# Optimization experiments

Hardware: AMD Instinct MI355X
Metric: run time of the kernel (lower is better)

The kernel has to match this reference:

```python
import jax, jax.numpy as jnp
import numpy as np

DIM = 768
D_STATE = 16
D_INNER = 2 * DIM  # expand=2


def setup_inputs() -> dict:
    key = jax.random.key(0)
    k_x, k_in, k_conv, k_out = jax.random.split(key, 4)
    B, L = 1, 4096
    x = jax.random.normal(k_x, (B, L, DIM), dtype=jnp.float32)
    # torch Linear weight layout: [out_features, in_features]
    W_in = jax.random.normal(k_in, (3 * D_INNER + 2 * D_STATE, DIM), dtype=jnp.float32) * 0.02
    # depthwise conv1d kernel: [out_ch=d_inner, in_ch/groups=1, k=3]
    W_conv = jax.random.normal(k_conv, (D_INNER, 1, 3), dtype=jnp.float32) * 0.1
    W_out = jax.random.normal(k_out, (DIM, D_INNER), dtype=jnp.float32) * 0.02
    A_log = jnp.log(jnp.tile(jnp.arange(1, D_STATE + 1, dtype=jnp.float32), (D_INNER, 1)))
    D = jnp.ones((D_INNER,), dtype=jnp.float32)
    return {"x": x, "W_in": W_in, "W_conv": W_conv, "W_out": W_out, "A_log": A_log, "D": D}


def reference(x, W_in, W_conv, W_out, A_log, D):
    d_inner = W_conv.shape[0]
    d_state = A_log.shape[1]
    Bsz = x.shape[0]

    xz = x @ W_in.T  # [B, L, 3*d_inner + 2*d_state]
    x_inner, z, B_ssm, C_ssm, delta = jnp.split(
        xz, [d_inner, 2 * d_inner, 2 * d_inner + d_state, 2 * d_inner + 2 * d_state], axis=-1
    )

    # depthwise conv over sequence: [B, d_inner, L]
    xc = jax.lax.conv_general_dilated(
        x_inner.transpose(0, 2, 1), W_conv,
        window_strides=(1,), padding=[(1, 1)], feature_group_count=d_inner,
    ).transpose(0, 2, 1)  # back to [B, L, d_inner]
    xc = jax.nn.silu(xc)

    A = -jnp.exp(A_log)  # [d_inner, d_state]
    delta = jax.nn.softplus(delta)  # [B, L, d_inner]
    dA = jnp.exp(jnp.einsum('bld,dn->bldn', delta, A))           # [B, L, d_inner, d_state]
    dBx = jnp.einsum('bld,bln,bld->bldn', delta, B_ssm, xc)      # delta_B * x fused

    def step(h, inp):
        da_t, dbx_t, c_t = inp  # [B,d,n], [B,d,n], [B,n]
        h = da_t * h + dbx_t
        y_t = jnp.einsum('bdn,bn->bd', h, c_t)
        return h, y_t

    h0 = jnp.zeros((Bsz, d_inner, d_state), dtype=x.dtype)
    _, ys = jax.lax.scan(
        step, h0,
        (dA.transpose(1, 0, 2, 3), dBx.transpose(1, 0, 2, 3), C_ssm.transpose(1, 0, 2)),
    )  # ys: [L, B, d_inner]

    y = ys.transpose(1, 0, 2) + xc * D  # skip connection
    y = y * jax.nn.silu(z)
    return y @ W_out.T  # [B, L, dim]
```

## Files before the change

### kernel.cpp

```cpp
#include <hip/hip_runtime.h>
#include <hip/hip_bf16.h>
#include <math.h>

#define LSEQ   4096
#define DIM    768
#define DINNER 1536
#define DSTATE 16
#define NCOLS  4640
#define NCH    128
#define CLEN   32
#define NPAD   4736

typedef _Float16 f16;
typedef __attribute__((ext_vector_type(8))) _Float16 f16x8;
typedef __attribute__((ext_vector_type(4))) float f32x4;

#define WSCALE   64.0f
#define WDESCALE 0.015625f

__device__ __forceinline__ void gld_lds16(void* lds_dst, const void* gsrc) {
    __builtin_amdgcn_global_load_lds(
        (__attribute__((address_space(1))) void*)(gsrc),
        (__attribute__((address_space(3))) void*)(lds_dst), 16, 0, 0);
}

template<int BM, int BN, int WM, int WN, int NTB, bool COLM, bool SPLIT, bool ZMODE>
__global__ __launch_bounds__(256) void gemm_f16(const f16* __restrict__ A,
                                                const f16* __restrict__ B,
                                                float* __restrict__ C,
                                                f16* __restrict__ Z,
                                                int M, int N, int K, int ldc,
                                                float cscale) {
    constexpr int MI  = WM / 16;
    constexpr int NI  = WN / 16;
    constexpr int NWN = BN / WN;
    constexpr int nA  = BM / 16;
    constexpr int nB  = BN / 16;
    constexpr int NPL = SPLIT ? 2 : 1;
    constexpr int NT  = nA + NPL * nB;

    __shared__ __align__(16) f16 As[BM * 32];
    __shared__ __align__(16) f16 Bs[NPL * BN * 32];

    const int P   = gridDim.x >> 3;
    const int idx = (blockIdx.x & 7) * P + (blockIdx.x >> 3);
    const int m0  = (COLM ? (idx % NTB) : (idx / NTB)) * BM;
    const int n0  = (COLM ? (idx / NTB) : (idx % NTB)) * BN;

    const int tid  = threadIdx.x;
    const int w    = tid >> 6;
    const int lane = tid & 63;
    const int wr   = w / NWN;
    const int wc   = w % NWN;
    const int m    = lane & 15;
    const int q    = lane >> 4;
    const int rsub = lane >> 2;
    const int bsel = lane & 3;
    const int ldb  = NPL * K;

    f32x4 acc[MI][NI];
#pragma unroll
    for (int i = 0; i < MI; i++)
#pragma unroll
        for (int j = 0; j < NI; j++) acc[i][j] = (f32x4){0.f, 0.f, 0.f, 0.f};

    const int fragoff = ((q ^ (m & 3)) << 3);

    for (int k0 = 0; k0 < K; k0 += 32) {
#pragma unroll
        for (int t = w; t < NT; t += 4) {
            const f16* g; f16* lb; int rl;
            if (t < nA) {
                rl = t * 16 + rsub;
                g  = A + (size_t)(m0 + rl) * K + k0 + (bsel ^ (rl & 3)) * 8;
                lb = As + t * 16 * 32;
            } else if (t < nA + nB) {
                int tt = t - nA; rl = tt * 16 + rsub;
                g  = B + (size_t)(n0 + rl) * ldb + k0 + (bsel ^ (rl & 3)) * 8;
                lb = Bs + tt * 16 * 32;
            } else {
                int tt = t - nA - nB; rl = tt * 16 + rsub;
                g  = B + (size_t)(n0 + rl) * ldb + K + k0 + (bsel ^ (rl & 3)) * 8;
                lb = Bs + (nB + tt) * 16 * 32;
            }
            gld_lds16(lb, g);
        }
        __syncthreads();

        f16x8 af[MI], bh[NI];
#pragma unroll
        for (int i = 0; i < MI; i++)
            af[i] = *(const f16x8*)&As[(wr * WM + i * 16 + m) * 32 + fragoff];
#pragma unroll
        for (int j = 0; j < NI; j++)
            bh[j] = *(const f16x8*)&Bs[(wc * WN + j * 16 + m) * 32 + fragoff];
#pragma unroll
        for (int i = 0; i < MI; i++)
#pragma unroll
            for (int j = 0; j < NI; j++)
                acc[i][j] = __builtin_amdgcn_mfma_f32_16x16x32_f16(af[i], bh[j], acc[i][j], 0, 0, 0);
        if (SPLIT) {
            f16x8 bl[NI];
#pragma unroll
            for (int j = 0; j < NI; j++)
                bl[j] = *(const f16x8*)&Bs[BN * 32 + (wc * WN + j * 16 + m) * 32 + fragoff];
#pragma unroll
            for (int i = 0; i < MI; i++)
#pragma unroll
                for (int j = 0; j < NI; j++)
                    acc[i][j] = __builtin_amdgcn_mfma_f32_16x16x32_f16(af[i], bl[j], acc[i][j], 0, 0, 0);
        }
        __syncthreads();
    }

    if (ZMODE && n0 >= DINNER && n0 < 2 * DINNER) {
#pragma unroll
        for (int i = 0; i < MI; i++) {
#pragma unroll
            for (int j = 0; j < NI; j++) {
                const int col = n0 - DINNER + wc * WN + j * 16 + m;
                const int rowb = m0 + wr * WM + i * 16 + q * 4;
#pragma unroll
                for (int r = 0; r < 4; r++)
                    Z[(size_t)(rowb + r) * DINNER + col] = (f16)acc[i][j][r];
            }
        }
        return;
    }
#pragma unroll
    for (int i = 0; i < MI; i++) {
#pragma unroll
        for (int j = 0; j < NI; j++) {
            const int col = n0 + wc * WN + j * 16 + m;
            if (col >= N) continue;
            const int rowb = m0 + wr * WM + i * 16 + q * 4;
#pragma unroll
            for (int r = 0; r < 4; r++)
                C[(size_t)(rowb + r) * ldc + col] = acc[i][j][r] * cscale;
        }
    }
}

#define E0 (LSEQ * DIM)
#define E1 (E0 + NPAD * DIM)
#define E2 (E1 + DIM * DINNER)

__global__ __launch_bounds__(256) void cvt_all(const float* __restrict__ x,
                                               const float* __restrict__ Wi,
                                               const float* __restrict__ Wo,
                                               f16* __restrict__ Ax,
                                               f16* __restrict__ Bw,
                                               f16* __restrict__ Bo) {
    int i = (blockIdx.x * 256 + threadIdx.x) * 4;
    if (i < E0) {
        float4 v = *(const float4*)(x + i);
        Ax[i] = (f16)v.x; Ax[i+1] = (f16)v.y; Ax[i+2] = (f16)v.z; Ax[i+3] = (f16)v.w;
    } else if (i < E1) {
        int e = i - E0;
        int n = e / DIM;
        if (n < NCOLS) {
            float4 v = *(const float4*)(Wi + e);
            Bw[e] = (f16)v.x; Bw[e+1] = (f16)v.y; Bw[e+2] = (f16)v.z; Bw[e+3] = (f16)v.w;
        } else {
            Bw[e] = (f16)0.f; Bw[e+1] = (f16)0.f; Bw[e+2] = (f16)0.f; Bw[e+3] = (f16)0.f;
        }
    } else if (i < E2) {
        int e = i - E1;
        int n = e / DINNER, k = e - n * DINNER;
        float4 v = *(const float4*)(Wo + e);
        float a[4] = {v.x * WSCALE, v.y * WSCALE, v.z * WSCALE, v.w * WSCALE};
        f16* row = Bo + (size_t)n * (2 * DINNER) + k;
#pragma unroll
        for (int j = 0; j < 4; j++) {
            f16 hi = (f16)a[j];
            row[j] = hi; row[DINNER + j] = (f16)(a[j] - (float)hi);
        }
    }
}

__global__ __launch_bounds__(256) void scan1_kernel(const float* __restrict__ xz,
                                                    const float* __restrict__ Wc,
                                                    const float* __restrict__ A_log,
                                                    float* __restrict__ aprod,
                                                    float* __restrict__ hend) {
    __shared__ float Bs[CLEN * DSTATE];
    const int d  = blockIdx.x * 256 + threadIdx.x;
    const int c  = blockIdx.y;
    const int l0 = c * CLEN;
    for (int i = threadIdx.x; i < CLEN * DSTATE; i += 256)
        Bs[i] = xz[(size_t)(l0 + (i >> 4)) * NCOLS + 3072 + (i & 15)];
    float Areg[DSTATE];
#pragma unroll
    for (int n = 0; n < DSTATE; n++) Areg[n] = -__expf(A_log[d * DSTATE + n]);
    const float w0 = Wc[d * 3 + 0], w1 = Wc[d * 3 + 1], w2 = Wc[d * 3 + 2];
    float xm = (l0 > 0) ? xz[(size_t)(l0 - 1) * NCOLS + d] : 0.f;
    float x0 = xz[(size_t)l0 * NCOLS + d];
    float ld_xp   = xz[(size_t)(l0 + 1) * NCOLS + d];
    float ld_draw = xz[(size_t)l0 * NCOLS + 3104 + d];
    __syncthreads();

    float h[DSTATE];
#pragma unroll
    for (int n = 0; n < DSTATE; n++) h[n] = 0.f;
    float S = 0.f;

    for (int t = 0; t < CLEN; t++) {
        const int l = l0 + t;
        float xp = ld_xp, draw = ld_draw;
        if (t + 1 < CLEN) {
            ld_xp   = (l + 2 < LSEQ) ? xz[(size_t)(l + 2) * NCOLS + d] : 0.f;
            ld_draw = xz[(size_t)(l + 1) * NCOLS + 3104 + d];
        }
        float v  = xm * w0 + x0 * w1 + xp * w2;
        float xcv = __fdividef(v, 1.f + __expf(-v));
        float dtv = (draw > 20.f) ? draw : __logf(1.f + __expf(draw));
        float u = dtv * xcv;
        S += dtv;
#pragma unroll
        for (int n = 0; n < DSTATE; n++) {
            float e = __expf(dtv * Areg[n]);
            h[n] = e * h[n] + u * Bs[t * DSTATE + n];
        }
        xm = x0; x0 = xp;
    }
#pragma unroll
    for (int n = 0; n < DSTATE; n++) {
        size_t idx = ((size_t)c * DSTATE + n) * DINNER + d;
        aprod[idx] = __expf(S * Areg[n]);
        hend[idx]  = h[n];
    }
}

__global__ __launch_bounds__(256) void scan2_kernel(const float* __restrict__ aprod,
                                                    const float* __restrict__ hend,
                                                    float* __restrict__ hinit) {
    const int g = blockIdx.x * 256 + threadIdx.x;
    const size_t S = (size_t)DSTATE * DINNER;
    size_t idx = g;
    float a = aprod[idx], e = hend[idx];
    float h = 0.f;
#pragma unroll 4
    for (int c = 0; c < NCH; c++) {
        float ac = a, ec = e;
        if (c + 1 < NCH) { a = aprod[idx + S]; e = hend[idx + S]; }
        hinit[idx] = h;
        h = ac * h + ec;
        idx += S;
    }
}

__global__ __launch_bounds__(256) void scan3_kernel(const float* __restrict__ xz,
                                                    const f16* __restrict__ Zb,
                                                    const float* __restrict__ Wc,
                                                    const float* __restrict__ A_log,
                                                    const float* __restrict__ hinit,
                                                    const float* __restrict__ Dp,
                                                    f16* __restrict__ Ay) {
    __shared__ float Bs[CLEN * DSTATE];
    __shared__ float Cs[CLEN * DSTATE];
    const int d  = blockIdx.x * 256 + threadIdx.x;
    const int c  = blockIdx.y;
    const int l0 = c * CLEN;
    for (int i = threadIdx.x; i < CLEN * DSTATE; i += 256) {
        size_t roff = (size_t)(l0 + (i >> 4)) * NCOLS;
        Bs[i] = xz[roff + 3072 + (i & 15)];
        Cs[i] = xz[roff + 3088 + (i & 15)];
    }
    float Areg[DSTATE];
#pragma unroll
    for (int n = 0; n < DSTATE; n++) Areg[n] = -__expf(A_log[d * DSTATE + n]);
    float h[DSTATE];
#pragma unroll
    for (int n = 0; n < DSTATE; n++)
        h[n] = hinit[((size_t)c * DSTATE + n) * DINNER + d];
    const float Dv = Dp[d];
    const float w0 = Wc[d * 3 + 0], w1 = Wc[d * 3 + 1], w2 = Wc[d * 3 + 2];
    float xm = (l0 > 0) ? xz[(size_t)(l0 - 1) * NCOLS + d] : 0.f;
    float x0 = xz[(size_t)l0 * NCOLS + d];
    float ld_xp   = xz[(size_t)(l0 + 1) * NCOLS + d];
    float ld_draw = xz[(size_t)l0 * NCOLS + 3104 + d];
    float ld_z    = (float)Zb[(size_t)l0 * DINNER + d];
    __syncthreads();

    for (int t = 0; t < CLEN; t++) {
        const int l = l0 + t;
        float xp = ld_xp, draw = ld_draw, zv = ld_z;
        if (t + 1 < CLEN) {
            ld_xp   = (l + 2 < LSEQ) ? xz[(size_t)(l + 2) * NCOLS + d] : 0.f;
            ld_draw = xz[(size_t)(l + 1) * NCOLS + 3104 + d];
            ld_z    = (float)Zb[(size_t)(l + 1) * DINNER + d];
        }
        float v  = xm * w0 + x0 * w1 + xp * w2;
        float xcv = __fdividef(v, 1.f + __expf(-v));
        float dtv = (draw > 20.f) ? draw : __logf(1.f + __expf(draw));
        float u = dtv * xcv;
        float y = 0.f;
#pragma unroll
        for (int n = 0; n < DSTATE; n++) {
            float e = __expf(dtv * Areg[n]);
            h[n] = e * h[n] + u * Bs[t * DSTATE + n];
            y += h[n] * Cs[t * DSTATE + n];
        }
        float sz = __fdividef(zv, 1.f + __expf(-zv));
        Ay[(size_t)l * DINNER + d] = (f16)((y + xcv * Dv) * sz);
        xm = x0; x0 = xp;
    }
}

extern "C" void kernel_launch(void* const* d_in, const int* in_sizes, int n_in,
                              void* d_out, int out_size, void* d_ws, size_t ws_size,
                              hipStream_t stream) {
    const float* x     = (const float*)d_in[0];
    const float* W_in  = (const float*)d_in[1];
    const float* W_conv= (const float*)d_in[2];
    const float* W_out = (const float*)d_in[3];
    const float* A_log = (const float*)d_in[4];
    const float* Dp    = (const float*)d_in[5];
    float* out = (float*)d_out;

    float* ws  = (float*)d_ws;
    float* xz  = ws;
    float* ap  = xz + (size_t)LSEQ * NCOLS;
    float* he  = ap + (size_t)NCH * DSTATE * DINNER;
    float* hi  = he + (size_t)NCH * DSTATE * DINNER;
    f16* Ax = (f16*)(hi + (size_t)NCH * DSTATE * DINNER);
    f16* Ay = Ax + (size_t)LSEQ * DIM;
    f16* Bw = Ay + (size_t)LSEQ * DINNER;
    f16* Bo = Bw + (size_t)NPAD * DIM;
    f16* Zb = Bo + (size_t)DIM * 2 * DINNER;

    cvt_all<<<E2 / 1024, 256, 0, stream>>>(x, W_in, W_out, Ax, Bw, Bo);

    gemm_f16<128, 128, 64, 64, 32, true, false, true><<<1184, 256, 0, stream>>>(
        Ax, Bw, xz, Zb, LSEQ, NCOLS, DIM, NCOLS, 1.0f);

    scan1_kernel<<<dim3(DINNER / 256, NCH), 256, 0, stream>>>(
        xz, W_conv, A_log, ap, he);
    scan2_kernel<<<(DINNER * DSTATE) / 256, 256, 0, stream>>>(ap, he, hi);
    scan3_kernel<<<dim3(DINNER / 256, NCH), 256, 0, stream>>>(
        xz, Zb, W_conv, A_log, hi, Dp, Ay);

    gemm_f16<64, 64, 32, 32, 12, false, true, false><<<768, 256, 0, stream>>>(
        Ay, Bo, out, nullptr, LSEQ, DIM, DINNER, DIM, WDESCALE);
}
```

Measured before the change: 265.1 us.

## Store x_inner as fp16, compact B/C/delta buffer, K=64 tiles, drop split-precision W_out

```diff
diff --git a/kernel.cpp b/kernel.cpp
--- a/kernel.cpp
+++ b/kernel.cpp
@@ -10,13 +10,11 @@
 #define NCH    128
 #define CLEN   32
 #define NPAD   4736
+#define DXW    1568
 
 typedef _Float16 f16;
 typedef __attribute__((ext_vector_type(8))) _Float16 f16x8;
 typedef __attribute__((ext_vector_type(4))) float f32x4;
-
-#define WSCALE   64.0f
-#define WDESCALE 0.015625f
 
 __device__ __forceinline__ void gld_lds16(void* lds_dst, const void* gsrc) {
     __builtin_amdgcn_global_load_lds(
@@ -24,23 +22,22 @@
         (__attribute__((address_space(3))) void*)(lds_dst), 16, 0, 0);
 }
 
-template<int BM, int BN, int WM, int WN, int NTB, bool COLM, bool SPLIT, bool ZMODE>
+template<int BM, int BN, int WM, int WN, int NTB, bool COLM, bool ZMODE>
 __global__ __launch_bounds__(256) void gemm_f16(const f16* __restrict__ A,
                                                 const f16* __restrict__ B,
                                                 float* __restrict__ C,
-                                                f16* __restrict__ Z,
-                                                int M, int N, int K, int ldc,
-                                                float cscale) {
+                                                f16* __restrict__ Xb,
+                                                f16* __restrict__ Zb,
+                                                int M, int N, int K, int ldc) {
     constexpr int MI  = WM / 16;
     constexpr int NI  = WN / 16;
     constexpr int NWN = BN / WN;
-    constexpr int nA  = BM / 16;
-    constexpr int nB  = BN / 16;
-    constexpr int NPL = SPLIT ? 2 : 1;
-    constexpr int NT  = nA + NPL * nB;
-
-    __shared__ __align__(16) f16 As[BM * 32];
-    __shared__ __align__(16) f16 Bs[NPL * BN * 32];
+    constexpr int RT  = BM + BN;
+    constexpr int NS  = RT / 8;
+
+    __shared__ __align__(16) f16 S[RT * 64];
+    f16* As = S;
+    f16* Bs = S + BM * 64;
 
     const int P   = gridDim.x >> 3;
     const int idx = (blockIdx.x & 7) * P + (blockIdx.x >> 3);
@@ -54,9 +51,8 @@
     const int wc   = w % NWN;
     const int m    = lane & 15;
     const int q    = lane >> 4;
-    const int rsub = lane >> 2;
-    const int bsel = lane & 3;
-    const int ldb  = NPL * K;
+    const int rl8  = lane >> 3;
+    const int bsel = lane & 7;
 
     f32x4 acc[MI][NI];
 #pragma unroll
@@ -64,81 +60,76 @@
 #pragma unroll
         for (int j = 0; j < NI; j++) acc[i][j] = (f32x4){0.f, 0.f, 0.f, 0.f};
 
-    const int fragoff = ((q ^ (m & 3)) << 3);
-
-    for (int k0 = 0; k0 < K; k0 += 32) {
-#pragma unroll
-        for (int t = w; t < NT; t += 4) {
-            const f16* g; f16* lb; int rl;
-            if (t < nA) {
-                rl = t * 16 + rsub;
-                g  = A + (size_t)(m0 + rl) * K + k0 + (bsel ^ (rl & 3)) * 8;
-                lb = As + t * 16 * 32;
-            } else if (t < nA + nB) {
-                int tt = t - nA; rl = tt * 16 + rsub;
-                g  = B + (size_t)(n0 + rl) * ldb + k0 + (bsel ^ (rl & 3)) * 8;
-                lb = Bs + tt * 16 * 32;
-            } else {
-                int tt = t - nA - nB; rl = tt * 16 + rsub;
-                g  = B + (size_t)(n0 + rl) * ldb + K + k0 + (bsel ^ (rl & 3)) * 8;
-                lb = Bs + (nB + tt) * 16 * 32;
+    for (int k0 = 0; k0 < K; k0 += 64) {
+#pragma unroll
+        for (int t = w; t < NS; t += 4) {
+            const int rl  = t * 8 + rl8;
+            const int blk = bsel ^ (rl & 7);
+            const f16* g = (rl < BM)
+                ? A + (size_t)(m0 + rl) * K + k0 + blk * 8
+                : B + (size_t)(n0 + rl - BM) * K + k0 + blk * 8;
+            gld_lds16(S + t * 8 * 64, g);
+        }
+        __syncthreads();
+
+#pragma unroll
+        for (int kk = 0; kk < 2; kk++) {
+            const int fo = (((q + 4 * kk) ^ (m & 7)) << 3);
+            f16x8 af[MI], bh[NI];
+#pragma unroll
+            for (int i = 0; i < MI; i++)
+                af[i] = *(const f16x8*)&As[(wr * WM + i * 16 + m) * 64 + fo];
+#pragma unroll
+            for (int j = 0; j < NI; j++)
+                bh[j] = *(const f16x8*)&Bs[(wc * WN + j * 16 + m) * 64 + fo];
+#pragma unroll
+            for (int i = 0; i < MI; i++)
+#pragma unroll
+                for (int j = 0; j < NI; j++)
+                    acc[i][j] = __builtin_amdgcn_mfma_f32_16x16x32_f16(
+                        af[i], bh[j], acc[i][j], 0, 0, 0);
+        }
+        __syncthreads();
+    }
+
+    if (ZMODE && n0 < DINNER) {
+#pragma unroll
+        for (int i = 0; i < MI; i++)
+#pragma unroll
+            for (int j = 0; j < NI; j++) {
+                const int col  = n0 + wc * WN + j * 16 + m;
+                const int rowb = m0 + wr * WM + i * 16 + q * 4;
+#pragma unroll
+                for (int r = 0; r < 4; r++)
+                    Xb[(size_t)(rowb + r) * DINNER + col] = (f16)acc[i][j][r];
             }
-            gld_lds16(lb, g);
-        }
-        __syncthreads();
-
-        f16x8 af[MI], bh[NI];
+        return;
+    }
+    if (ZMODE && n0 < 2 * DINNER) {
 #pragma unroll
         for (int i = 0; i < MI; i++)
-            af[i] = *(const f16x8*)&As[(wr * WM + i * 16 + m) * 32 + fragoff];
-#pragma unroll
-        for (int j = 0; j < NI; j++)
-            bh[j] = *(const f16x8*)&Bs[(wc * WN + j * 16 + m) * 32 + fragoff];
-#pragma unroll
-        for (int i = 0; i < MI; i++)
-#pragma unroll
-            for (int j = 0; j < NI; j++)
-                acc[i][j] = __builtin_amdgcn_mfma_f32_16x16x32_f16(af[i], bh[j], acc[i][j], 0, 0, 0);
-        if (SPLIT) {
-            f16x8 bl[NI];
-#pragma unroll
-            for (int j = 0; j < NI; j++)
-                bl[j] = *(const f16x8*)&Bs[BN * 32 + (wc * WN + j * 16 + m) * 32 + fragoff];
-#pragma unroll
-            for (int i = 0; i < MI; i++)
-#pragma unroll
-                for (int j = 0; j < NI; j++)
-                    acc[i][j] = __builtin_amdgcn_mfma_f32_16x16x32_f16(af[i], bl[j], acc[i][j], 0, 0, 0);
-        }
-        __syncthreads();
-    }
-
-    if (ZMODE && n0 >= DINNER && n0 < 2 * DINNER) {
-#pragma unroll
-        for (int i = 0; i < MI; i++) {
 #pragma unroll
             for (int j = 0; j < NI; j++) {
-                const int col = n0 - DINNER + wc * WN + j * 16 + m;
+                const int col  = n0 - DINNER + wc * WN + j * 16 + m;
                 const int rowb = m0 + wr * WM + i * 16 + q * 4;
 #pragma unroll
                 for (int r = 0; r < 4; r++)
-                    Z[(size_t)(rowb + r) * DINNER + col] = (f16)acc[i][j][r];
+                    Zb[(size_t)(rowb + r) * DINNER + col] = (f16)acc[i][j][r];
             }
-        }
         return;
     }
 #pragma unroll
-    for (int i = 0; i < MI; i++) {
+    for (int i = 0; i < MI; i++)
 #pragma unroll
         for (int j = 0; j < NI; j++) {
-            const int col = n0 + wc * WN + j * 16 + m;
-            if (col >= N) continue;
+            const int col  = (ZMODE ? n0 - 2 * DINNER : n0) + wc * WN + j * 16 + m;
+            const int lim  = ZMODE ? DXW : N;
+            if (col >= lim) continue;
             const int rowb = m0 + wr * WM + i * 16 + q * 4;
 #pragma unroll
             for (int r = 0; r < 4; r++)
-                C[(size_t)(rowb + r) * ldc + col] = acc[i][j][r] * cscale;
-        }
-    }
+                C[(size_t)(rowb + r) * ldc + col] = acc[i][j][r];
+        }
 }
 
 #define E0 (LSEQ * DIM)
@@ -166,19 +157,13 @@
         }
     } else if (i < E2) {
         int e = i - E1;
-        int n = e / DINNER, k = e - n * DINNER;
         float4 v = *(const float4*)(Wo + e);
-        float a[4] = {v.x * WSCALE, v.y * WSCALE, v.z * WSCALE, v.w * WSCALE};
-        f16* row = Bo + (size_t)n * (2 * DINNER) + k;
-#pragma unroll
-        for (int j = 0; j < 4; j++) {
-            f16 hi = (f16)a[j];
-            row[j] = hi; row[DINNER + j] = (f16)(a[j] - (float)hi);
-        }
-    }
-}
-
-__global__ __launch_bounds__(256) void scan1_kernel(const float* __restrict__ xz,
+        Bo[e] = (f16)v.x; Bo[e+1] = (f16)v.y; Bo[e+2] = (f16)v.z; Bo[e+3] = (f16)v.w;
+    }
+}
+
+__global__ __launch_bounds__(256) void scan1_kernel(const float* __restrict__ Dxz,
+                                                    const f16* __restrict__ Xb,
                                                     const float* __restrict__ Wc,
                                                     const float* __restrict__ A_log,
                                                     float* __restrict__ aprod,
@@ -188,15 +173,15 @@
     const int c  = blockIdx.y;
     const int l0 = c * CLEN;
     for (int i = threadIdx.x; i < CLEN * DSTATE; i += 256)
-        Bs[i] = xz[(size_t)(l0 + (i >> 4)) * NCOLS + 3072 + (i & 15)];
+        Bs[i] = Dxz[(size_t)(l0 + (i >> 4)) * DXW + (i & 15)];
     float Areg[DSTATE];
 #pragma unroll
     for (int n = 0; n < DSTATE; n++) Areg[n] = -__expf(A_log[d * DSTATE + n]);
     const float w0 = Wc[d * 3 + 0], w1 = Wc[d * 3 + 1], w2 = Wc[d * 3 + 2];
-    float xm = (l0 > 0) ? xz[(size_t)(l0 - 1) * NCOLS + d] : 0.f;
-    float x0 = xz[(size_t)l0 * NCOLS + d];
-    float ld_xp   = xz[(size_t)(l0 + 1) * NCOLS + d];
-    float ld_draw = xz[(size_t)l0 * NCOLS + 3104 + d];
+    float xm = (l0 > 0) ? (float)Xb[(size_t)(l0 - 1) * DINNER + d] : 0.f;
+    float x0 = (float)Xb[(size_t)l0 * DINNER + d];
+    float ld_xp   = (float)Xb[(size_t)(l0 + 1) * DINNER + d];
+    float ld_draw = Dxz[(size_t)l0 * DXW + 32 + d];
     __syncthreads();
 
     float h[DSTATE];
@@ -208,8 +193,8 @@
         const int l = l0 + t;
         float xp = ld_xp, draw = ld_draw;
         if (t + 1 < CLEN) {
-            ld_xp   = (l + 2 < LSEQ) ? xz[(size_t)(l + 2) * NCOLS + d] : 0.f;
-            ld_draw = xz[(size_t)(l + 1) * NCOLS + 3104 + d];
+            ld_xp   = (l + 2 < LSEQ) ? (float)Xb[(size_t)(l + 2) * DINNER + d] : 0.f;
+            ld_draw = Dxz[(size_t)(l + 1) * DXW + 32 + d];
         }
         float v  = xm * w0 + x0 * w1 + xp * w2;
         float xcv = __fdividef(v, 1.f + __expf(-v));
@@ -249,7 +234,8 @@
     }
 }
 
-__global__ __launch_bounds__(256) void scan3_kernel(const float* __restrict__ xz,
+__global__ __launch_bounds__(256) void scan3_kernel(const float* __restrict__ Dxz,
+                                                    const f16* __restrict__ Xb,
                                                     const f16* __restrict__ Zb,
                                                     const float* __restrict__ Wc,
                                                     const float* __restrict__ A_log,
@@ -262,9 +248,9 @@
     const int c  = blockIdx.y;
     const int l0 = c * CLEN;
     for (int i = threadIdx.x; i < CLEN * DSTATE; i += 256) {
-        size_t roff = (size_t)(l0 + (i >> 4)) * NCOLS;
-        Bs[i] = xz[roff + 3072 + (i & 15)];
-        Cs[i] = xz[roff + 3088 + (i & 15)];
+        size_t roff = (size_t)(l0 + (i >> 4)) * DXW;
+        Bs[i] = Dxz[roff + (i & 15)];
+        Cs[i] = Dxz[roff + 16 + (i & 15)];
     }
     float Areg[DSTATE];
 #pragma unroll
@@ -275,10 +261,10 @@
         h[n] = hinit[((size_t)c * DSTATE + n) * DINNER + d];
     const float Dv = Dp[d];
     const float w0 = Wc[d * 3 + 0], w1 = Wc[d * 3 + 1], w2 = Wc[d * 3 + 2];
-    float xm = (l0 > 0) ? xz[(size_t)(l0 - 1) * NCOLS + d] : 0.f;
-    float x0 = xz[(size_t)l0 * NCOLS + d];
-    float ld_xp   = xz[(size_t)(l0 + 1) * NCOLS + d];
-    float ld_draw = xz[(size_t)l0 * NCOLS + 3104 + d];
+    float xm = (l0 > 0) ? (float)Xb[(size_t)(l0 - 1) * DINNER + d] : 0.f;
+    float x0 = (float)Xb[(size_t)l0 * DINNER + d];
+    float ld_xp   = (float)Xb[(size_t)(l0 + 1) * DINNER + d];
+    float ld_draw = Dxz[(size_t)l0 * DXW + 32 + d];
     float ld_z    = (float)Zb[(size_t)l0 * DINNER + d];
     __syncthreads();
 
@@ -286,8 +272,8 @@
         const int l = l0 + t;
         float xp = ld_xp, draw = ld_draw, zv = ld_z;
         if (t + 1 < CLEN) {
-            ld_xp   = (l + 2 < LSEQ) ? xz[(size_t)(l + 2) * NCOLS + d] : 0.f;
-            ld_draw = xz[(size_t)(l + 1) * NCOLS + 3104 + d];
+            ld_xp   = (l + 2 < LSEQ) ? (float)Xb[(size_t)(l + 2) * DINNER + d] : 0.f;
+            ld_draw = Dxz[(size_t)(l + 1) * DXW + 32 + d];
             ld_z    = (float)Zb[(size_t)(l + 1) * DINNER + d];
         }
         float v  = xm * w0 + x0 * w1 + xp * w2;
@@ -319,27 +305,28 @@
     float* out = (float*)d_out;
 
     float* ws  = (float*)d_ws;
-    float* xz  = ws;
-    float* ap  = xz + (size_t)LSEQ * NCOLS;
+    float* Dxz = ws;
+    float* ap  = Dxz + (size_t)LSEQ * DXW;
     float* he  = ap + (size_t)NCH * DSTATE * DINNER;
     float* hi  = he + (size_t)NCH * DSTATE * DINNER;
     f16* Ax = (f16*)(hi + (size_t)NCH * DSTATE * DINNER);
     f16* Ay = Ax + (size_t)LSEQ * DIM;
     f16* Bw = Ay + (size_t)LSEQ * DINNER;
     f16* Bo = Bw + (size_t)NPAD * DIM;
-    f16* Zb = Bo + (size_t)DIM * 2 * DINNER;
+    f16* Zb = Bo + (size_t)DIM * DINNER;
+    f16* Xb = Zb + (size_t)LSEQ * DINNER;
 
     cvt_all<<<E2 / 1024, 256, 0, stream>>>(x, W_in, W_out, Ax, Bw, Bo);
 
-    gemm_f16<128, 128, 64, 64, 32, true, false, true><<<1184, 256, 0, stream>>>(
-        Ax, Bw, xz, Zb, LSEQ, NCOLS, DIM, NCOLS, 1.0f);
+    gemm_f16<128, 128, 64, 64, 32, true, true><<<1184, 256, 0, stream>>>(
+        Ax, Bw, Dxz, Xb, Zb, LSEQ, NCOLS, DIM, DXW);
 
     scan1_kernel<<<dim3(DINNER / 256, NCH), 256, 0, stream>>>(
-        xz, W_conv, A_log, ap, he);
+        Dxz, Xb, W_conv, A_log, ap, he);
     scan2_kernel<<<(DINNER * DSTATE) / 256, 256, 0, stream>>>(ap, he, hi);
     scan3_kernel<<<dim3(DINNER / 256, NCH), 256, 0, stream>>>(
-        xz, Zb, W_conv, A_log, hi, Dp, Ay);
-
-    gemm_f16<64, 64, 32, 32, 12, false, true, false><<<768, 256, 0, stream>>>(
-        Ay, Bo, out, nullptr, LSEQ, DIM, DINNER, DIM, WDESCALE);
-}
+        Dxz, Xb, Zb, W_conv, A_log, hi, Dp, Ay);
+
+    gemm_f16<64, 64, 32, 32, 12, false, false><<<768, 256, 0, stream>>>(
+        Ay, Bo, out, nullptr, nullptr, LSEQ, DIM, DINNER, DIM);
+}
```

After: 246.6 us. 1.07x faster.
